# Kernel optimization log

Measured on AMD Instinct MI355X. Metric: run time of the kernel, lower is better.

The kernel has to match this reference:

```python
import jax, jax.numpy as jnp
import numpy as np
from jax import lax


def setup_inputs() -> dict:
    key = jax.random.key(0)
    k1, k2 = jax.random.split(key)
    B, H, W, C = 8, 32, 32, 512
    N = 16384
    feature_batch = jax.random.normal(k1, (B, H, W, C), dtype=jnp.float32)
    mb = jax.random.normal(k2, (N, C), dtype=jnp.float32)
    return {"feature_batch": feature_batch, "mb": mb, "b": 9}


def reference(feature_batch, mb, b):
    B, H, W, C = feature_batch.shape
    fv = feature_batch.reshape(B * H * W, C)                       # (Q, C)
    sq = (
        jnp.sum(fv * fv, axis=1)[:, None]
        + jnp.sum(mb * mb, axis=1)[None, :]
        - 2.0 * (fv @ mb.T)
    )                                                               # (Q, N)
    sq = jnp.maximum(sq, 0.0)  # guard fp round-off before sqrt
    # smallest-b distances, sorted ascending (top_k of negated values)
    neg_topk = lax.top_k(-sq, b)[0]                                 # (Q, b)
    top_k_dists_squared = -neg_topk
    pixel_scores = jnp.sqrt(top_k_dists_squared[:, 0]).reshape(B, H * W)
    max_idx = jnp.argmax(pixel_scores, axis=1)                      # (B,)
    softmax_args = jnp.sqrt(
        top_k_dists_squared.reshape(B, H * W, b)[jnp.arange(B), max_idx, :]
    )                                                               # (B, b)
    image_scores = softmax_args[:, 0]
    if b > 1:
        image_scores = image_scores * (1.0 - jax.nn.softmax(softmax_args, axis=1)[:, 0])
    pixel_scores = pixel_scores.reshape(B, 1, H, W)
    return pixel_scores, image_scores
```

## Files before the change

### kernel.cpp

```cpp
#include <hip/hip_runtime.h>

typedef unsigned short u16;

#define M_ROWS 8192
#define N_ROWS 16384
#define KDIM   512
#define BM     256
#define BN     128
#define BK     32
#define NCHUNKS 16
#define NPER   (N_ROWS / NCHUNKS)
#define TOPK   9

#define ASZ (BM * BK)
#define BSZ (BN * BK)
#define NTT ((NPER / BN) * (KDIM / BK))

typedef __attribute__((ext_vector_type(8)))  short bf16x8;
typedef __attribute__((ext_vector_type(16))) float f32x16;

__device__ __forceinline__ void gload_lds16(const void* g, void* l) {
  __builtin_amdgcn_global_load_lds(
      (const __attribute__((address_space(1))) void*)g,
      (__attribute__((address_space(3))) void*)l,
      16, 0, 0);
}

__device__ __forceinline__ u16 f2bf(float x) {
  union { float f; unsigned u; } c; c.f = x;
  unsigned u = c.u;
  u += 0x7fffu + ((u >> 16) & 1u);
  return (u16)(u >> 16);
}

__device__ __forceinline__ void topk_update(float v, float* best) {
  if (v < best[TOPK - 1]) {
    #pragma unroll
    for (int i = 0; i < TOPK; ++i) {
      float b = best[i];
      best[i] = fminf(b, v);
      v = fmaxf(b, v);
    }
  }
}

__global__ __launch_bounds__(256) void prep_kernel(
    const float* __restrict__ fv, const float* __restrict__ mb,
    u16* __restrict__ fvb, u16* __restrict__ mbb,
    float* __restrict__ nf, float* __restrict__ nm_perm)
{
  int idx = blockIdx.x * 4 + (threadIdx.x >> 6);
  int l = threadIdx.x & 63;
  const float* src; u16* dst;
  if (idx < M_ROWS) {
    src = fv + (size_t)idx * KDIM; dst = fvb + (size_t)idx * KDIM;
  } else {
    int r = idx - M_ROWS;
    src = mb + (size_t)r * KDIM; dst = mbb + (size_t)r * KDIM;
  }
  float4 x0 = ((const float4*)src)[2 * l];
  float4 x1 = ((const float4*)src)[2 * l + 1];
  float s = x0.x * x0.x + x0.y * x0.y + x0.z * x0.z + x0.w * x0.w
          + x1.x * x1.x + x1.y * x1.y + x1.z * x1.z + x1.w * x1.w;
  uint4 o;
  o.x = (unsigned)f2bf(x0.x) | ((unsigned)f2bf(x0.y) << 16);
  o.y = (unsigned)f2bf(x0.z) | ((unsigned)f2bf(x0.w) << 16);
  o.z = (unsigned)f2bf(x1.x) | ((unsigned)f2bf(x1.y) << 16);
  o.w = (unsigned)f2bf(x1.z) | ((unsigned)f2bf(x1.w) << 16);
  ((uint4*)dst)[l] = o;
  #pragma unroll
  for (int off = 32; off > 0; off >>= 1) s += __shfl_down(s, off, 64);
  if (l == 0) {
    if (idx < M_ROWS) {
      nf[idx] = s;
    } else {
      int n  = idx - M_ROWS;
      int ig = n >> 5;
      int w5 = n & 31;
      int h  = (w5 >> 2) & 1;
      int r  = (w5 & 3) | ((w5 >> 3) << 2);
      nm_perm[(ig * 2 + h) * 16 + r] = s;
    }
  }
}

__global__ __launch_bounds__(256, 2) void gemm_topk_kernel(
    const u16* __restrict__ fvb, const u16* __restrict__ mbb,
    const float* __restrict__ nm_perm, float* __restrict__ partial)
{
  extern __shared__ __align__(16) u16 sm[];
  u16* const Asm = sm;
  u16* const Bsm = sm + 3 * ASZ;

  const int t   = threadIdx.x;
  const int l   = t & 63;
  const int w   = t >> 6;
  const int h   = l >> 5;
  const int c31 = l & 31;
  const int xr  = (c31 >> 1) & 3;

  const int m0    = blockIdx.x * BM;
  const int ncoff = blockIdx.y * NPER;

  const int srow = l >> 2;
  const int sc   = ((l & 3) ^ ((l >> 3) & 3)) * 8;

  const u16* aSrc = fvb + (size_t)(m0 + w * 64 + srow) * KDIM + sc;
  const u16* bSrc = mbb + (size_t)(ncoff + w * 32 + srow) * KDIM + sc;

  const int aRd  = (w * 64 + c31) * BK;
  const int ch0  = (h ^ xr) * 8;
  const int ch1  = ch0 ^ 16;

#define STAGE(kc2_, bufS_) do {                                               \
    const size_t ao_ = (size_t)((kc2_) & 15) * BK;                            \
    const size_t so_ = (size_t)((kc2_) >> 4) * ((size_t)BN * KDIM) + ao_;     \
    u16* ad_ = Asm + (bufS_) * ASZ + (w * 64) * BK;                           \
    u16* bd_ = Bsm + (bufS_) * BSZ + (w * 32) * BK;                           \
    gload_lds16(aSrc + ao_,                 ad_);                             \
    gload_lds16(aSrc + ao_ + 16 * KDIM,     ad_ + 16 * BK);                   \
    gload_lds16(aSrc + ao_ + 32 * KDIM,     ad_ + 32 * BK);                   \
    gload_lds16(aSrc + ao_ + 48 * KDIM,     ad_ + 48 * BK);                   \
    gload_lds16(bSrc + so_,                 bd_);                             \
    gload_lds16(bSrc + so_ + 16 * KDIM,     bd_ + 16 * BK);                   \
  } while (0)

  float best[2][TOPK];
  float T[2];
  #pragma unroll
  for (int s = 0; s < 2; ++s) {
    T[s] = 3.4e38f;
    #pragma unroll
    for (int i = 0; i < TOPK; ++i) best[s][i] = 3.4e38f;
  }

  f32x16 acc[2][4];

  STAGE(0, 0);
  STAGE(1, 1);
  asm volatile("s_waitcnt vmcnt(6)" ::: "memory");
  __builtin_amdgcn_s_barrier();

  int bC = 0, bS = 2;
  for (int tt = 0; tt < NTT; ++tt) {
    if ((tt & 15) == 0) {
      #pragma unroll
      for (int s = 0; s < 2; ++s)
        #pragma unroll
        for (int i = 0; i < 4; ++i)
          #pragma unroll
          for (int r = 0; r < 16; ++r) acc[s][i][r] = 0.0f;
    }

    const int kc2 = tt + 2;
    if (kc2 < NTT) STAGE(kc2, bS);

    {
      const u16* Ak = Asm + bC * ASZ;
      const u16* Bk = Bsm + bC * BSZ;
      {
        bf16x8 f0 = *(const bf16x8*)&Ak[aRd + ch0];
        bf16x8 f1 = *(const bf16x8*)&Ak[aRd + 32 * BK + ch0];
        #pragma unroll
        for (int i = 0; i < 4; ++i) {
          bf16x8 mbf = *(const bf16x8*)&Bk[(i * 32 + c31) * BK + ch0];
          acc[0][i] = __builtin_amdgcn_mfma_f32_32x32x16_bf16(mbf, f0, acc[0][i], 0, 0, 0);
          acc[1][i] = __builtin_amdgcn_mfma_f32_32x32x16_bf16(mbf, f1, acc[1][i], 0, 0, 0);
        }
      }
      {
        bf16x8 f0 = *(const bf16x8*)&Ak[aRd + ch1];
        bf16x8 f1 = *(const bf16x8*)&Ak[aRd + 32 * BK + ch1];
        #pragma unroll
        for (int i = 0; i < 4; ++i) {
          bf16x8 mbf = *(const bf16x8*)&Bk[(i * 32 + c31) * BK + ch1];
          acc[0][i] = __builtin_amdgcn_mfma_f32_32x32x16_bf16(mbf, f0, acc[0][i], 0, 0, 0);
          acc[1][i] = __builtin_amdgcn_mfma_f32_32x32x16_bf16(mbf, f1, acc[1][i], 0, 0, 0);
        }
      }
    }

    if (tt < NTT - 1) {
      if (tt < NTT - 2) { asm volatile("s_waitcnt vmcnt(6)" ::: "memory"); }
      else              { asm volatile("s_waitcnt vmcnt(0)" ::: "memory"); }
      __builtin_amdgcn_s_barrier();
    }

    if ((tt & 15) == 15) {
      const int nt    = tt >> 4;
      const int nbase = ncoff + nt * BN;
      #pragma unroll
      for (int i = 0; i < 4; ++i) {
        const float4* np = (const float4*)&nm_perm[(((nbase >> 5) + i) * 2 + h) * 16];
        float4 q0 = np[0], q1 = np[1], q2 = np[2], q3 = np[3];
        #pragma unroll
        for (int s = 0; s < 2; ++s) {
          float v[16];
          v[ 0] = fmaf(-2.0f, acc[s][i][ 0], q0.x);
          v[ 1] = fmaf(-2.0f, acc[s][i][ 1], q0.y);
          v[ 2] = fmaf(-2.0f, acc[s][i][ 2], q0.z);
          v[ 3] = fmaf(-2.0f, acc[s][i][ 3], q0.w);
          v[ 4] = fmaf(-2.0f, acc[s][i][ 4], q1.x);
          v[ 5] = fmaf(-2.0f, acc[s][i][ 5], q1.y);
          v[ 6] = fmaf(-2.0f, acc[s][i][ 6], q1.z);
          v[ 7] = fmaf(-2.0f, acc[s][i][ 7], q1.w);
          v[ 8] = fmaf(-2.0f, acc[s][i][ 8], q2.x);
          v[ 9] = fmaf(-2.0f, acc[s][i][ 9], q2.y);
          v[10] = fmaf(-2.0f, acc[s][i][10], q2.z);
          v[11] = fmaf(-2.0f, acc[s][i][11], q2.w);
          v[12] = fmaf(-2.0f, acc[s][i][12], q3.x);
          v[13] = fmaf(-2.0f, acc[s][i][13], q3.y);
          v[14] = fmaf(-2.0f, acc[s][i][14], q3.z);
          v[15] = fmaf(-2.0f, acc[s][i][15], q3.w);
          float bmin = 3.4e38f;
          #pragma unroll
          for (int r = 0; r < 16; ++r) bmin = fminf(bmin, v[r]);
          if (bmin < T[s]) {
            #pragma unroll
            for (int r = 0; r < 16; ++r) topk_update(v[r], best[s]);
            T[s] = best[s][TOPK - 1];
          }
        }
      }
      #pragma unroll
      for (int s = 0; s < 2; ++s)
        T[s] = fminf(best[s][TOPK - 1], __shfl_xor(best[s][TOPK - 1], 32, 64));
    }

    bC = (bC == 2) ? 0 : bC + 1;
    bS = (bS == 2) ? 0 : bS + 1;
  }

  #pragma unroll
  for (int s = 0; s < 2; ++s) {
    float tmp[TOPK];
    #pragma unroll
    for (int q = 0; q < TOPK; ++q) tmp[q] = __shfl_xor(best[s][q], 32, 64);
    #pragma unroll
    for (int q = 0; q < TOPK; ++q) topk_update(tmp[q], best[s]);
    int m = m0 + w * 64 + s * 32 + c31;
    size_t base = ((size_t)blockIdx.y * M_ROWS + m) * TOPK;
    if (h == 0) {
      #pragma unroll
      for (int q = 0; q < 5; ++q) partial[base + q] = best[s][q];
    } else {
      #pragma unroll
      for (int q = 5; q < TOPK; ++q) partial[base + q] = best[s][q];
    }
  }
}

__global__ __launch_bounds__(256) void merge_kernel(
    const float* __restrict__ partial, const float* __restrict__ nf,
    float* __restrict__ final9, float* __restrict__ out_pix)
{
  int row = blockIdx.x * 256 + threadIdx.x;
  float best[TOPK];
  #pragma unroll
  for (int i = 0; i < TOPK; ++i) best[i] = 3.4e38f;
  for (int s = 0; s < NCHUNKS; ++s) {
    const float* p = &partial[((size_t)s * M_ROWS + row) * TOPK];
    #pragma unroll
    for (int i = 0; i < TOPK; ++i) topk_update(p[i], best);
  }
  float nfr = nf[row];
  float d[TOPK];
  #pragma unroll
  for (int i = 0; i < TOPK; ++i) d[i] = sqrtf(fmaxf(best[i] + nfr, 0.0f));
  out_pix[row] = d[0];
  #pragma unroll
  for (int i = 0; i < TOPK; ++i) final9[(size_t)row * TOPK + i] = d[i];
}

__global__ __launch_bounds__(256) void img_kernel(
    const float* __restrict__ out_pix, const float* __restrict__ final9,
    const int* __restrict__ bptr, float* __restrict__ out_img)
{
  int img = blockIdx.x, t = threadIdx.x;
  float bv = -1.0f; int bi = 0;
  for (int p = t; p < 1024; p += 256) {
    float v = out_pix[img * 1024 + p];
    if (v > bv) { bv = v; bi = p; }
  }
  __shared__ float sv[256];
  __shared__ int   si[256];
  sv[t] = bv; si[t] = bi;
  __syncthreads();
  for (int off = 128; off > 0; off >>= 1) {
    if (t < off) {
      float v2 = sv[t + off]; int i2 = si[t + off];
      if (v2 > sv[t] || (v2 == sv[t] && i2 < si[t])) { sv[t] = v2; si[t] = i2; }
    }
    __syncthreads();
  }
  if (t == 0) {
    int row = img * 1024 + si[0];
    int b = bptr[0];
    float s0 = final9[(size_t)row * TOPK + 0];
    float score = s0;
    if (b > 1) {
      int bb = b < TOPK ? b : TOPK;
      float mx = s0;
      for (int i = 1; i < bb; ++i) mx = fmaxf(mx, final9[(size_t)row * TOPK + i]);
      float den = 0.0f;
      for (int i = 0; i < bb; ++i) den += expf(final9[(size_t)row * TOPK + i] - mx);
      score = s0 * (1.0f - expf(s0 - mx) / den);
    }
    out_img[img] = score;
  }
}

extern "C" void kernel_launch(void* const* d_in, const int* in_sizes, int n_in,
                              void* d_out, int out_size, void* d_ws, size_t ws_size,
                              hipStream_t stream) {
  const float* fv   = (const float*)d_in[0];
  const float* mb   = (const float*)d_in[1];
  const int*   bptr = (const int*)d_in[2];
  float* out = (float*)d_out;

  char* ws = (char*)d_ws;
  u16*   fvb     = (u16*)ws;
  u16*   mbb     = (u16*)(ws + 8388608);
  float* nf      = (float*)(ws + 25165824);
  float* nm_perm = (float*)(ws + 25198592);
  float* partial = (float*)(ws + 25264128);
  float* final9  = (float*)(ws + 29982720);

  hipLaunchKernelGGL(prep_kernel, dim3((M_ROWS + N_ROWS) / 4), dim3(256), 0, stream,
                     fv, mb, fvb, mbb, nf, nm_perm);
  hipLaunchKernelGGL(gemm_topk_kernel, dim3(M_ROWS / BM, NCHUNKS), dim3(256),
                     73728, stream, fvb, mbb, nm_perm, partial);
  hipLaunchKernelGGL(merge_kernel, dim3(M_ROWS / 256), dim3(256), 0, stream,
                     partial, nf, final9, out);
  hipLaunchKernelGGL(img_kernel, dim3(8), dim3(256), 0, stream,
                     out, final9, bptr, out + M_ROWS);
}
```

Measured before the change: 312.6 us.

## Split k-step into two phases interleaving staged loads with MFMA bursts

Restructures the main loop so each 32-wide k-tile runs as two half-steps. Each half-step preloads all LDS fragments, issues half of the next tile's global-to-LDS copies (A in the first, B in the second), barriers, then runs its 8 MFMAs under raised wave priority via s_setprio. The staging index moves from a recomputed kc2 to incrementing ko2/nOff2 counters. The goal is to spread global-load issue across the compute and keep waves in lockstep so MFMA bursts overlap memory traffic, at the cost of two extra barriers per iteration.

```diff
diff --git a/kernel.cpp b/kernel.cpp
--- a/kernel.cpp
+++ b/kernel.cpp
@@ -109,20 +109,23 @@
   const u16* bSrc = mbb + (size_t)(ncoff + w * 32 + srow) * KDIM + sc;
 
   const int aRd  = (w * 64 + c31) * BK;
+  const int bRd  = c31 * BK;
   const int ch0  = (h ^ xr) * 8;
   const int ch1  = ch0 ^ 16;
 
-#define STAGE(kc2_, bufS_) do {                                               \
-    const size_t ao_ = (size_t)((kc2_) & 15) * BK;                            \
-    const size_t so_ = (size_t)((kc2_) >> 4) * ((size_t)BN * KDIM) + ao_;     \
+#define STAGE_A(koS_, bufS_) do {                                             \
+    const size_t ao_ = (size_t)(koS_) * BK;                                   \
     u16* ad_ = Asm + (bufS_) * ASZ + (w * 64) * BK;                           \
+    gload_lds16(aSrc + ao_,             ad_);                                 \
+    gload_lds16(aSrc + ao_ + 16 * KDIM, ad_ + 16 * BK);                       \
+    gload_lds16(aSrc + ao_ + 32 * KDIM, ad_ + 32 * BK);                       \
+    gload_lds16(aSrc + ao_ + 48 * KDIM, ad_ + 48 * BK);                       \
+  } while (0)
+#define STAGE_B(koS_, nOffS_, bufS_) do {                                     \
+    const size_t bo_ = (size_t)(nOffS_) + (size_t)(koS_) * BK;                \
     u16* bd_ = Bsm + (bufS_) * BSZ + (w * 32) * BK;                           \
-    gload_lds16(aSrc + ao_,                 ad_);                             \
-    gload_lds16(aSrc + ao_ + 16 * KDIM,     ad_ + 16 * BK);                   \
-    gload_lds16(aSrc + ao_ + 32 * KDIM,     ad_ + 32 * BK);                   \
-    gload_lds16(aSrc + ao_ + 48 * KDIM,     ad_ + 48 * BK);                   \
-    gload_lds16(bSrc + so_,                 bd_);                             \
-    gload_lds16(bSrc + so_ + 16 * KDIM,     bd_ + 16 * BK);                   \
+    gload_lds16(bSrc + bo_,             bd_);                                 \
+    gload_lds16(bSrc + bo_ + 16 * KDIM, bd_ + 16 * BK);                       \
   } while (0)
 
   float best[2][TOPK];
@@ -136,12 +139,14 @@
 
   f32x16 acc[2][4];
 
-  STAGE(0, 0);
-  STAGE(1, 1);
+  STAGE_A(0, 0); STAGE_B(0, 0, 0);
+  STAGE_A(1, 1); STAGE_B(1, 0, 1);
   asm volatile("s_waitcnt vmcnt(6)" ::: "memory");
   __builtin_amdgcn_s_barrier();
 
   int bC = 0, bS = 2;
+  int ko2 = 2;
+  int nOff2 = 0;
   for (int tt = 0; tt < NTT; ++tt) {
     if ((tt & 15) == 0) {
       #pragma unroll
@@ -152,38 +157,58 @@
           for (int r = 0; r < 16; ++r) acc[s][i][r] = 0.0f;
     }
 
-    const int kc2 = tt + 2;
-    if (kc2 < NTT) STAGE(kc2, bS);
+    const u16* Ak = Asm + bC * ASZ;
+    const u16* Bk = Bsm + bC * BSZ;
+    const bool doStage = (tt + 2 < NTT);
 
     {
-      const u16* Ak = Asm + bC * ASZ;
-      const u16* Bk = Bsm + bC * BSZ;
-      {
-        bf16x8 f0 = *(const bf16x8*)&Ak[aRd + ch0];
-        bf16x8 f1 = *(const bf16x8*)&Ak[aRd + 32 * BK + ch0];
-        #pragma unroll
-        for (int i = 0; i < 4; ++i) {
-          bf16x8 mbf = *(const bf16x8*)&Bk[(i * 32 + c31) * BK + ch0];
-          acc[0][i] = __builtin_amdgcn_mfma_f32_32x32x16_bf16(mbf, f0, acc[0][i], 0, 0, 0);
-          acc[1][i] = __builtin_amdgcn_mfma_f32_32x32x16_bf16(mbf, f1, acc[1][i], 0, 0, 0);
-        }
+      bf16x8 f0 = *(const bf16x8*)&Ak[aRd + ch0];
+      bf16x8 f1 = *(const bf16x8*)&Ak[aRd + 1024 + ch0];
+      bf16x8 g0 = *(const bf16x8*)&Bk[bRd +    0 + ch0];
+      bf16x8 g1 = *(const bf16x8*)&Bk[bRd + 1024 + ch0];
+      bf16x8 g2 = *(const bf16x8*)&Bk[bRd + 2048 + ch0];
+      bf16x8 g3 = *(const bf16x8*)&Bk[bRd + 3072 + ch0];
+      if (doStage) STAGE_A(ko2, bS);
+      __builtin_amdgcn_s_barrier();
+      asm volatile("s_waitcnt lgkmcnt(0)" ::: "memory");
+      __builtin_amdgcn_s_setprio(1);
+      acc[0][0] = __builtin_amdgcn_mfma_f32_32x32x16_bf16(g0, f0, acc[0][0], 0, 0, 0);
+      acc[1][0] = __builtin_amdgcn_mfma_f32_32x32x16_bf16(g0, f1, acc[1][0], 0, 0, 0);
+      acc[0][1] = __builtin_amdgcn_mfma_f32_32x32x16_bf16(g1, f0, acc[0][1], 0, 0, 0);
+      acc[1][1] = __builtin_amdgcn_mfma_f32_32x32x16_bf16(g1, f1, acc[1][1], 0, 0, 0);
+      acc[0][2] = __builtin_amdgcn_mfma_f32_32x32x16_bf16(g2, f0, acc[0][2], 0, 0, 0);
+      acc[1][2] = __builtin_amdgcn_mfma_f32_32x32x16_bf16(g2, f1, acc[1][2], 0, 0, 0);
+      acc[0][3] = __builtin_amdgcn_mfma_f32_32x32x16_bf16(g3, f0, acc[0][3], 0, 0, 0);
+      acc[1][3] = __builtin_amdgcn_mfma_f32_32x32x16_bf16(g3, f1, acc[1][3], 0, 0, 0);
+      __builtin_amdgcn_s_setprio(0);
+      __builtin_amdgcn_s_barrier();
+    }
+
+    {
+      bf16x8 f0 = *(const bf16x8*)&Ak[aRd + ch1];
+      bf16x8 f1 = *(const bf16x8*)&Ak[aRd + 1024 + ch1];
+      bf16x8 g0 = *(const bf16x8*)&Bk[bRd +    0 + ch1];
+      bf16x8 g1 = *(const bf16x8*)&Bk[bRd + 1024 + ch1];
+      bf16x8 g2 = *(const bf16x8*)&Bk[bRd + 2048 + ch1];
+      bf16x8 g3 = *(const bf16x8*)&Bk[bRd + 3072 + ch1];
+      if (doStage) STAGE_B(ko2, nOff2, bS);
+      __builtin_amdgcn_s_barrier();
+      asm volatile("s_waitcnt lgkmcnt(0)" ::: "memory");
+      __builtin_amdgcn_s_setprio(1);
+      acc[0][0] = __builtin_amdgcn_mfma_f32_32x32x16_bf16(g0, f0, acc[0][0], 0, 0, 0);
+      acc[1][0] = __builtin_amdgcn_mfma_f32_32x32x16_bf16(g0, f1, acc[1][0], 0, 0, 0);
+      acc[0][1] = __builtin_amdgcn_mfma_f32_32x32x16_bf16(g1, f0, acc[0][1], 0, 0, 0);
+      acc[1][1] = __builtin_amdgcn_mfma_f32_32x32x16_bf16(g1, f1, acc[1][1], 0, 0, 0);
+      acc[0][2] = __builtin_amdgcn_mfma_f32_32x32x16_bf16(g2, f0, acc[0][2], 0, 0, 0);
+      acc[1][2] = __builtin_amdgcn_mfma_f32_32x32x16_bf16(g2, f1, acc[1][2], 0, 0, 0);
+      acc[0][3] = __builtin_amdgcn_mfma_f32_32x32x16_bf16(g3, f0, acc[0][3], 0, 0, 0);
+      acc[1][3] = __builtin_amdgcn_mfma_f32_32x32x16_bf16(g3, f1, acc[1][3], 0, 0, 0);
+      __builtin_amdgcn_s_setprio(0);
+      if (tt < NTT - 1) {
+        if (tt < NTT - 2) { asm volatile("s_waitcnt vmcnt(6)" ::: "memory"); }
+        else              { asm volatile("s_waitcnt vmcnt(0)" ::: "memory"); }
+        __builtin_amdgcn_s_barrier();
       }
-      {
-        bf16x8 f0 = *(const bf16x8*)&Ak[aRd + ch1];
-        bf16x8 f1 = *(const bf16x8*)&Ak[aRd + 32 * BK + ch1];
-        #pragma unroll
-        for (int i = 0; i < 4; ++i) {
-          bf16x8 mbf = *(const bf16x8*)&Bk[(i * 32 + c31) * BK + ch1];
-          acc[0][i] = __builtin_amdgcn_mfma_f32_32x32x16_bf16(mbf, f0, acc[0][i], 0, 0, 0);
-          acc[1][i] = __builtin_amdgcn_mfma_f32_32x32x16_bf16(mbf, f1, acc[1][i], 0, 0, 0);
-        }
-      }
-    }
-
-    if (tt < NTT - 1) {
-      if (tt < NTT - 2) { asm volatile("s_waitcnt vmcnt(6)" ::: "memory"); }
-      else              { asm volatile("s_waitcnt vmcnt(0)" ::: "memory"); }
-      __builtin_amdgcn_s_barrier();
     }
 
     if ((tt & 15) == 15) {
@@ -229,6 +254,7 @@
 
     bC = (bC == 2) ? 0 : bC + 1;
     bS = (bS == 2) ? 0 : bS + 1;
+    if (ko2 == 15) { ko2 = 0; nOff2 += BN * KDIM; } else { ++ko2; }
   }
 
   #pragma unroll
```

Result: slower. 319.6 us (+2.2%).
